# Performance work log

Measured on AMD Instinct MI355X. Metric: run time of the kernel, lower is better.

## Reference

```python
import jax, jax.numpy as jnp
import numpy as np


def setup_inputs() -> dict:
    key = jax.random.key(0)
    ks = jax.random.split(key, 5)
    bsz, input_size, hidden_size, level_hidden = 8192, 1024, 1024, 64
    d_in = input_size + hidden_size
    return {
        "input": jax.random.normal(ks[0], (bsz, input_size), dtype=jnp.float32),
        "h_prev": jax.random.normal(ks[1], (bsz, hidden_size), dtype=jnp.float32),
        "c_prev": jax.random.normal(ks[2], (bsz, hidden_size), dtype=jnp.float32),
        "W_lstm": jax.random.normal(ks[3], (4 * hidden_size, d_in), dtype=jnp.float32) * (1.0 / np.sqrt(d_in)),
        "W_level": jax.random.normal(ks[4], (2 * level_hidden, d_in), dtype=jnp.float32) * (1.0 / np.sqrt(d_in)),
    }


def reference(input, h_prev, c_prev, W_lstm, W_level):
    hidden_size = h_prev.shape[1]
    level_hidden = W_level.shape[0] // 2
    n_repeat = hidden_size // level_hidden

    combined = jnp.concatenate([input, h_prev], axis=-1)  # (B, in+hid)
    lstm_out = combined @ W_lstm.T                        # (B, 4*hid)
    cc_i, cc_f, cc_o, cc_g = jnp.split(lstm_out, 4, axis=1)
    level_out = combined @ W_level.T                      # (B, 2*lvl)
    cc_i_h, cc_f_h = jnp.split(level_out, 2, axis=1)

    i = jax.nn.sigmoid(cc_i)
    f = jax.nn.sigmoid(cc_f)
    o = jax.nn.sigmoid(cc_o)
    g = jnp.tanh(cc_g)

    p_f = jax.nn.softmax(cc_f_h, axis=-1)
    p_i = jax.nn.softmax(cc_i_h, axis=-1)
    f_h = jnp.cumsum(p_f, axis=-1)                         # forward cumsum
    i_h = jnp.flip(jnp.cumsum(jnp.flip(p_i, -1), axis=-1), -1)  # reverse cumsum

    # expand each level gate value across its chunk of the hidden dim
    i_h = jnp.repeat(i_h, n_repeat, axis=1)                # (B, hid)
    f_h = jnp.repeat(f_h, n_repeat, axis=1)

    w = i_h * f_h
    c = w * (f * c_prev + i * g) + (f_h - w) * c_prev + (i_h - w) * g
    h = o * jnp.tanh(c)
    return (h, c)
```

## Files before the change

### kernel.cpp

```cpp
#include <hip/hip_runtime.h>


typedef unsigned short u16;
typedef __attribute__((ext_vector_type(8))) short bf16x8;
typedef __attribute__((ext_vector_type(8))) short s8v;
typedef __attribute__((ext_vector_type(4))) float f32x4;
typedef __attribute__((ext_vector_type(4))) float v4f;

#define GLDS(g, l) __builtin_amdgcn_global_load_lds(                      \
    (const __attribute__((address_space(1))) void*)(g),                   \
    (__attribute__((address_space(3))) void*)(l), 16, 0, 0)

__device__ __forceinline__ u16 f2bf(float x) {
  unsigned u = __builtin_bit_cast(unsigned, x);
  u += 0x7FFFu + ((u >> 16) & 1u);
  return (u16)(u >> 16);
}
__device__ __forceinline__ float bf2f(u16 h) {
  unsigned u = ((unsigned)h) << 16;
  return __builtin_bit_cast(float, u);
}
__device__ __forceinline__ float fsig(float x) { return 1.0f / (1.0f + __expf(-x)); }
__device__ __forceinline__ float ftanhf(float x) { float e = __expf(2.0f * x); return 1.0f - 2.0f / (e + 1.0f); }

__global__ __launch_bounds__(256) void k_convert(
    const float* __restrict__ inp, const float* __restrict__ hprev,
    const float* __restrict__ wl, const float* __restrict__ wlev,
    u16* __restrict__ Ahi, u16* __restrict__ Alo,
    u16* __restrict__ Whi, u16* __restrict__ Wlo)
{
  const int GA = (8192 * 2048) / 8;
  const int GW = (4224 * 2048) / 8;
  for (int gi = blockIdx.x * 256 + threadIdx.x; gi < GA + GW; gi += gridDim.x * 256) {
    if (gi < GA) {
      int e = gi << 3; int row = e >> 11, col = e & 2047;
      const float* src = (col < 1024) ? (inp + row * 1024 + col)
                                      : (hprev + row * 1024 + (col - 1024));
      v4f a = *(const v4f*)src, b = *(const v4f*)(src + 4);
      float vv[8] = {a.x, a.y, a.z, a.w, b.x, b.y, b.z, b.w};
      s8v hi, lo;
#pragma unroll
      for (int j = 0; j < 8; ++j) {
        u16 h = f2bf(vv[j]);
        hi[j] = (short)h;
        lo[j] = (short)f2bf(vv[j] - bf2f(h));
      }
      *(s8v*)(Ahi + e) = hi;
      *(s8v*)(Alo + e) = lo;
    } else {
      int e = (gi - GA) << 3; int n = e >> 11, k = e & 2047;
      const float* src;
      if (n < 4096) { int j = n >> 2, g = n & 3; src = wl + (size_t)((g << 10) | j) * 2048 + k; }
      else          { src = wlev + (size_t)(n - 4096) * 2048 + k; }
      v4f a = *(const v4f*)src, b = *(const v4f*)(src + 4);
      float vv[8] = {a.x, a.y, a.z, a.w, b.x, b.y, b.z, b.w};
      s8v hi, lo;
#pragma unroll
      for (int j = 0; j < 8; ++j) {
        u16 h = f2bf(vv[j]);
        hi[j] = (short)h;
        lo[j] = (short)f2bf(vv[j] - bf2f(h));
      }
      *(s8v*)(Whi + e) = hi;
      if (n >= 4096) *(s8v*)(Wlo + (size_t)(n - 4096) * 2048 + k) = lo;
    }
  }
}

__global__ __launch_bounds__(256) void k_gemm_level(
    const u16* __restrict__ Ahi, const u16* __restrict__ Alo,
    const u16* __restrict__ Whi, const u16* __restrict__ Wlo,
    float* __restrict__ part)
{
  __shared__ __align__(16) u16 smem[4 * 8192];
  u16 *Ah = smem, *Al = smem + 8192, *Bh = smem + 16384, *Bl = smem + 24576;
  const int tid = threadIdx.x, lane = tid & 63, wid = tid >> 6;
  const int wm = wid >> 1, wn = wid & 1;
  const int rm = blockIdx.x, s = blockIdx.y;
  const int lrow = lane >> 3, lcolE = (lane & 7) << 3;
  const int c16 = lane & 15, r16 = lane >> 4;
  f32x4 acc[4][4] = {};
  const u16* aBaseH = Ahi + (size_t)(rm << 7) * 2048;
  const u16* aBaseL = Alo + (size_t)(rm << 7) * 2048;
  const u16* bBaseH = Whi + (size_t)4096 * 2048;

  for (int kt = 0; kt < 4; ++kt) {
    const int k0 = (s << 8) + (kt << 6);
#pragma unroll
    for (int q = 0; q < 4; ++q) {
      const int ca = (wid << 2) + q;
      size_t roff = (size_t)((ca << 3) + lrow) * 2048 + k0 + lcolE;
      GLDS(aBaseH + roff, Ah + (ca << 9));
      GLDS(aBaseL + roff, Al + (ca << 9));
      GLDS(bBaseH + roff, Bh + (ca << 9));
      GLDS(Wlo + roff,    Bl + (ca << 9));
    }
    __syncthreads();
#pragma unroll
    for (int ks = 0; ks < 2; ++ks) {
      bf16x8 ah[4], al[4];
#pragma unroll
      for (int i = 0; i < 4; ++i) {
        int off = ((wm << 6) + (i << 4) + c16) * 64 + (ks << 5) + (r16 << 3);
        ah[i] = *(const bf16x8*)(Ah + off);
        al[i] = *(const bf16x8*)(Al + off);
      }
#pragma unroll
      for (int j = 0; j < 4; ++j) {
        int off = ((wn << 6) + (j << 4) + c16) * 64 + (ks << 5) + (r16 << 3);
        bf16x8 bh = *(const bf16x8*)(Bh + off);
        bf16x8 bl = *(const bf16x8*)(Bl + off);
#pragma unroll
        for (int i = 0; i < 4; ++i) {
          acc[i][j] = __builtin_amdgcn_mfma_f32_16x16x32_bf16(ah[i], bh, acc[i][j], 0, 0, 0);
          acc[i][j] = __builtin_amdgcn_mfma_f32_16x16x32_bf16(al[i], bh, acc[i][j], 0, 0, 0);
          acc[i][j] = __builtin_amdgcn_mfma_f32_16x16x32_bf16(ah[i], bl, acc[i][j], 0, 0, 0);
        }
      }
    }
    __syncthreads();
  }
#pragma unroll
  for (int mi = 0; mi < 4; ++mi)
#pragma unroll
    for (int ni = 0; ni < 4; ++ni)
#pragma unroll
      for (int r = 0; r < 4; ++r) {
        int ml = (wm << 6) + (mi << 4) + (r16 << 2) + r;
        int nl = (wn << 6) + (ni << 4) + c16;
        part[(size_t)((s << 13) + (rm << 7) + ml) * 128 + nl] = acc[mi][ni][r];
      }
}

__global__ __launch_bounds__(256) void k_softmax(
    const float* __restrict__ part, float* __restrict__ ih, float* __restrict__ fh)
{
  const int tid = threadIdx.x, lane = tid & 63, w = tid >> 6;
  const int row = blockIdx.x * 4 + w;
  float vi = 0.f, vf = 0.f;
#pragma unroll
  for (int s = 0; s < 8; ++s) {
    vi += part[(size_t)((s << 13) + row) * 128 + lane];
    vf += part[(size_t)((s << 13) + row) * 128 + 64 + lane];
  }
  float mi = vi, mf = vf;
#pragma unroll
  for (int d = 1; d < 64; d <<= 1) {
    mi = fmaxf(mi, __shfl_xor(mi, d, 64));
    mf = fmaxf(mf, __shfl_xor(mf, d, 64));
  }
  float ei = __expf(vi - mi), ef = __expf(vf - mf);
  float si = ei, sf = ef;
#pragma unroll
  for (int d = 1; d < 64; d <<= 1) {
    si += __shfl_xor(si, d, 64);
    sf += __shfl_xor(sf, d, 64);
  }
  float pi = ei / si, pf = ef / sf;
  float ci = pi, cf = pf;
#pragma unroll
  for (int d = 1; d < 64; d <<= 1) {
    float t = __shfl_up(ci, d, 64); if (lane >= d) ci += t;
    float u = __shfl_up(cf, d, 64); if (lane >= d) cf += u;
  }
  ih[(row << 6) + lane] = 1.0f - (ci - pi);
  fh[(row << 6) + lane] = cf;
}

__global__ __launch_bounds__(512, 4) void k_gemm_main(
    const u16* __restrict__ Ab, const u16* __restrict__ Wb,
    const float* __restrict__ cprev, const float* __restrict__ ihp,
    const float* __restrict__ fhp, float* __restrict__ out)
{
  __shared__ __align__(16) u16 smem[36864];
  const int tid = threadIdx.x, lane = tid & 63, wid = tid >> 6;
  const int wm = wid >> 2, wn = wid & 3;
  const int c16 = lane & 15, r16 = lane >> 4;

  const int bx = blockIdx.x;
  const int nb = (bx & 7) * 128 + (bx >> 3);
  const int rm = nb >> 5, cm = nb & 31;

  const int sr = tid >> 2;
  const int slq = tid & 3;
  const int xk = (slq ^ ((sr >> 1) & 3)) << 3;
  const u16* pa = Ab + (size_t)(rm * 256 + sr) * 2048 + xk;
  const u16* pb = Wb + (size_t)(cm * 128 + sr) * 2048 + xk;
  char* const ldsW = (char*)smem + (wid << 10);

  const int xsl = (r16 ^ ((c16 >> 1) & 3)) << 3;
  const int base_a = (wm * 128 + c16) * 32 + xsl;
  const int base_b = 8192 + (wn * 32 + c16) * 32 + xsl;

  f32x4 acc[8][2] = {};

#define STAGE3(slice, slot) do {                                       \
    const u16* sa_ = pa + (slice) * 32;                                \
    const u16* sb_ = pb + (slice) * 32;                                \
    char* d_ = ldsW + (slot) * 24576;                                  \
    GLDS(sa_, d_); GLDS(sa_ + 262144, d_ + 8192);                      \
    GLDS(sb_, d_ + 16384);                                             \
  } while (0)

#define SLICE(s, slot, dostage) do {                                   \
    bf16x8 aX[8], bS[2];                                               \
    _Pragma("unroll")                                                  \
    for (int i = 0; i < 8; ++i)                                        \
      aX[i] = *(const bf16x8*)(smem + (slot) * 12288 + base_a + i * 512); \
    _Pragma("unroll")                                                  \
    for (int j = 0; j < 2; ++j)                                        \
      bS[j] = *(const bf16x8*)(smem + (slot) * 12288 + base_b + j * 512); \
    if (dostage) STAGE3(((s) + 2) & 63, ((s) + 2) % 3);                \
    asm volatile("s_waitcnt vmcnt(3)" ::: "memory");                   \
    __builtin_amdgcn_s_barrier();                                      \
    asm volatile("s_waitcnt lgkmcnt(0)" ::: "memory");                 \
    _Pragma("unroll")                                                  \
    for (int i = 0; i < 8; ++i)                                        \
      _Pragma("unroll")                                                \
      for (int j = 0; j < 2; ++j)                                      \
        acc[i][j] = __builtin_amdgcn_mfma_f32_16x16x32_bf16(           \
            aX[i], bS[j], acc[i][j], 0, 0, 0);                         \
    __builtin_amdgcn_s_barrier();                                      \
  } while (0)

  STAGE3(0, 0); STAGE3(1, 1);
  asm volatile("s_waitcnt vmcnt(3)" ::: "memory");
  __builtin_amdgcn_s_barrier();

  for (int u = 0; u < 21; ++u) {
    const int s0 = u * 3;
    SLICE(s0 + 0, 0, 1);
    SLICE(s0 + 1, 1, 1);
    SLICE(s0 + 2, 2, 1);
  }
  SLICE(63, 0, 0);
#undef SLICE
#undef STAGE3

  asm volatile("s_waitcnt vmcnt(0)" ::: "memory");
  __builtin_amdgcn_s_barrier();

  float* epi = (float*)smem;
#define EPIPASS(p) do {                                                \
    if (wm == (p)) {                                                   \
      _Pragma("unroll")                                                \
      for (int i = 0; i < 8; ++i)                                      \
        _Pragma("unroll")                                              \
        for (int j = 0; j < 2; ++j)                                    \
          _Pragma("unroll")                                            \
          for (int r = 0; r < 4; ++r) {                                \
            float v = acc[i][j][r];                                    \
            v = ((c16 & 3) == 3) ? ftanhf(v) : fsig(v);                \
            epi[(i * 16 + r16 * 4 + r) * 128 + wn * 32 + j * 16 + c16] = v; \
          }                                                            \
    }                                                                  \
    __syncthreads();                                                   \
    _Pragma("unroll")                                                  \
    for (int e = 0; e < 2; ++e) {                                      \
      int idx = (e << 9) + tid;                                        \
      int mrow = idx >> 3, q = idx & 7;                                \
      const float* g4 = epi + mrow * 128 + q * 16;                     \
      int rowg = rm * 256 + (p) * 128 + mrow;                          \
      int jgb = cm * 32 + q * 4;                                       \
      int lv = jgb >> 4;                                               \
      float vih = ihp[(rowg << 6) + lv], vfh = fhp[(rowg << 6) + lv];  \
      float wq = vih * vfh;                                            \
      v4f cp4 = *(const v4f*)(cprev + rowg * 1024 + jgb);              \
      float cpv[4] = {cp4.x, cp4.y, cp4.z, cp4.w};                     \
      v4f hv, cv;                                                      \
      _Pragma("unroll")                                                \
      for (int t = 0; t < 4; ++t) {                                    \
        v4f g = *(const v4f*)(g4 + t * 4);                             \
        float iv = g.x, fv = g.y, ov = g.z, gv = g.w;                  \
        float cpx = cpv[t];                                            \
        float c = wq * (fv * cpx + iv * gv) + (vfh - wq) * cpx + (vih - wq) * gv; \
        float h = ov * ftanhf(c);                                      \
        hv[t] = h; cv[t] = c;                                          \
      }                                                                \
      *(v4f*)(out + rowg * 1024 + jgb) = hv;                           \
      *(v4f*)(out + 8388608 + rowg * 1024 + jgb) = cv;                 \
    }                                                                  \
    __syncthreads();                                                   \
  } while (0)
  EPIPASS(0); EPIPASS(1);
#undef EPIPASS
}

extern "C" void kernel_launch(void* const* d_in, const int* in_sizes, int n_in,
                              void* d_out, int out_size, void* d_ws, size_t ws_size,
                              hipStream_t stream) {
  (void)in_sizes; (void)n_in; (void)out_size; (void)ws_size;
  const float* inp   = (const float*)d_in[0];
  const float* hprev = (const float*)d_in[1];
  const float* cprev = (const float*)d_in[2];
  const float* wl    = (const float*)d_in[3];
  const float* wlev  = (const float*)d_in[4];
  float* out = (float*)d_out;
  char* ws = (char*)d_ws;

  u16* Ahi  = (u16*)(ws);
  u16* Alo  = (u16*)(ws + 33554432);
  u16* Whi  = (u16*)(ws + 67108864);
  u16* Wlo  = (u16*)(ws + 84410368);
  float* part = (float*)(ws + 84934656);
  float* ih   = (float*)(ws + 118489088);
  float* fh   = (float*)(ws + 120586240);

  k_convert<<<dim3(2048), dim3(256), 0, stream>>>(inp, hprev, wl, wlev, Ahi, Alo, Whi, Wlo);
  k_gemm_level<<<dim3(64, 8), dim3(256), 0, stream>>>(Ahi, Alo, Whi, Wlo, part);
  k_softmax<<<dim3(2048), dim3(256), 0, stream>>>(part, ih, fh);
  k_gemm_main<<<dim3(1024), dim3(512), 0, stream>>>(Ahi, Whi, cprev, ih, fh, out);
}
```

Measured before the change: 224.2 us.

## Use 4-wave blocks with 128x64 warp tiles and double-buffered LDS register reads

Halves the main GEMM's threads per block from 512 to 256 and doubles each wave's tile to 8x4 MFMA blocks, so each A fragment read from LDS feeds four MFMAs instead of two. The loop is rewritten with two register sets (X/Y) so LDS reads for the next slice are issued before the MFMAs on the current slice, and each thread now issues six global-to-LDS loads per stage. This raises register pressure (64 accumulator vectors plus two fragment sets) and lowers waves per block, which risks spills or lower occupancy.

Measured after the change: 245.0 us. 1.09x slower.

```diff
diff --git a/kernel.cpp b/kernel.cpp
--- a/kernel.cpp
+++ b/kernel.cpp
@@ -167,14 +167,14 @@
   fh[(row << 6) + lane] = cf;
 }
 
-__global__ __launch_bounds__(512, 4) void k_gemm_main(
+__global__ __launch_bounds__(256, 2) void k_gemm_main(
     const u16* __restrict__ Ab, const u16* __restrict__ Wb,
     const float* __restrict__ cprev, const float* __restrict__ ihp,
     const float* __restrict__ fhp, float* __restrict__ out)
 {
   __shared__ __align__(16) u16 smem[36864];
   const int tid = threadIdx.x, lane = tid & 63, wid = tid >> 6;
-  const int wm = wid >> 2, wn = wid & 3;
+  const int wm = wid >> 1, wn = wid & 1;
   const int c16 = lane & 15, r16 = lane >> 4;
 
   const int bx = blockIdx.x;
@@ -190,55 +190,106 @@
 
   const int xsl = (r16 ^ ((c16 >> 1) & 3)) << 3;
   const int base_a = (wm * 128 + c16) * 32 + xsl;
-  const int base_b = 8192 + (wn * 32 + c16) * 32 + xsl;
-
-  f32x4 acc[8][2] = {};
-
-#define STAGE3(slice, slot) do {                                       \
+  const int base_b = 8192 + (wn * 64 + c16) * 32 + xsl;
+
+  f32x4 acc[8][4] = {};
+  bf16x8 aX0, aX1, aX2, aX3, aX4, aX5, aX6, aX7, bX0, bX1, bX2, bX3;
+  bf16x8 aY0, aY1, aY2, aY3, aY4, aY5, aY6, aY7, bY0, bY1, bY2, bY3;
+
+#define STAGE6(slice, slot) do {                                       \
     const u16* sa_ = pa + (slice) * 32;                                \
     const u16* sb_ = pb + (slice) * 32;                                \
     char* d_ = ldsW + (slot) * 24576;                                  \
-    GLDS(sa_, d_); GLDS(sa_ + 262144, d_ + 8192);                      \
-    GLDS(sb_, d_ + 16384);                                             \
-  } while (0)
-
-#define SLICE(s, slot, dostage) do {                                   \
-    bf16x8 aX[8], bS[2];                                               \
-    _Pragma("unroll")                                                  \
-    for (int i = 0; i < 8; ++i)                                        \
-      aX[i] = *(const bf16x8*)(smem + (slot) * 12288 + base_a + i * 512); \
-    _Pragma("unroll")                                                  \
-    for (int j = 0; j < 2; ++j)                                        \
-      bS[j] = *(const bf16x8*)(smem + (slot) * 12288 + base_b + j * 512); \
-    if (dostage) STAGE3(((s) + 2) & 63, ((s) + 2) % 3);                \
-    asm volatile("s_waitcnt vmcnt(3)" ::: "memory");                   \
-    __builtin_amdgcn_s_barrier();                                      \
-    asm volatile("s_waitcnt lgkmcnt(0)" ::: "memory");                 \
-    _Pragma("unroll")                                                  \
-    for (int i = 0; i < 8; ++i)                                        \
-      _Pragma("unroll")                                                \
-      for (int j = 0; j < 2; ++j)                                      \
-        acc[i][j] = __builtin_amdgcn_mfma_f32_16x16x32_bf16(           \
-            aX[i], bS[j], acc[i][j], 0, 0, 0);                         \
-    __builtin_amdgcn_s_barrier();                                      \
-  } while (0)
-
-  STAGE3(0, 0); STAGE3(1, 1);
-  asm volatile("s_waitcnt vmcnt(3)" ::: "memory");
-  __builtin_amdgcn_s_barrier();
-
-  for (int u = 0; u < 21; ++u) {
-    const int s0 = u * 3;
-    SLICE(s0 + 0, 0, 1);
-    SLICE(s0 + 1, 1, 1);
-    SLICE(s0 + 2, 2, 1);
-  }
-  SLICE(63, 0, 0);
-#undef SLICE
-#undef STAGE3
-
-  asm volatile("s_waitcnt vmcnt(0)" ::: "memory");
-  __builtin_amdgcn_s_barrier();
+    GLDS(sa_,          d_);                                            \
+    GLDS(sa_ + 131072, d_ + 4096);                                     \
+    GLDS(sa_ + 262144, d_ + 8192);                                     \
+    GLDS(sa_ + 393216, d_ + 12288);                                    \
+    GLDS(sb_,          d_ + 16384);                                    \
+    GLDS(sb_ + 131072, d_ + 20480);                                    \
+  } while (0)
+
+#define READX(slot) do {                                               \
+    const u16* p_ = smem + (slot) * 12288;                             \
+    aX0 = *(const bf16x8*)(p_ + base_a);                               \
+    aX1 = *(const bf16x8*)(p_ + base_a + 512);                         \
+    aX2 = *(const bf16x8*)(p_ + base_a + 1024);                        \
+    aX3 = *(const bf16x8*)(p_ + base_a + 1536);                        \
+    aX4 = *(const bf16x8*)(p_ + base_a + 2048);                        \
+    aX5 = *(const bf16x8*)(p_ + base_a + 2560);                        \
+    aX6 = *(const bf16x8*)(p_ + base_a + 3072);                        \
+    aX7 = *(const bf16x8*)(p_ + base_a + 3584);                        \
+    bX0 = *(const bf16x8*)(p_ + base_b);                               \
+    bX1 = *(const bf16x8*)(p_ + base_b + 512);                         \
+    bX2 = *(const bf16x8*)(p_ + base_b + 1024);                        \
+    bX3 = *(const bf16x8*)(p_ + base_b + 1536);                        \
+  } while (0)
+
+#define READY(slot) do {                                               \
+    const u16* p_ = smem + (slot) * 12288;                             \
+    aY0 = *(const bf16x8*)(p_ + base_a);                               \
+    aY1 = *(const bf16x8*)(p_ + base_a + 512);                         \
+    aY2 = *(const bf16x8*)(p_ + base_a + 1024);                        \
+    aY3 = *(const bf16x8*)(p_ + base_a + 1536);                        \
+    aY4 = *(const bf16x8*)(p_ + base_a + 2048);                        \
+    aY5 = *(const bf16x8*)(p_ + base_a + 2560);                        \
+    aY6 = *(const bf16x8*)(p_ + base_a + 3072);                        \
+    aY7 = *(const bf16x8*)(p_ + base_a + 3584);                        \
+    bY0 = *(const bf16x8*)(p_ + base_b);                               \
+    bY1 = *(const bf16x8*)(p_ + base_b + 512);                         \
+    bY2 = *(const bf16x8*)(p_ + base_b + 1024);                        \
+    bY3 = *(const bf16x8*)(p_ + base_b + 1536);                        \
+  } while (0)
+
+#define MM1(i_, A_)                                                    \
+    acc[i_][0] = __builtin_amdgcn_mfma_f32_16x16x32_bf16(A_, b_0, acc[i_][0], 0, 0, 0); \
+    acc[i_][1] = __builtin_amdgcn_mfma_f32_16x16x32_bf16(A_, b_1, acc[i_][1], 0, 0, 0); \
+    acc[i_][2] = __builtin_amdgcn_mfma_f32_16x16x32_bf16(A_, b_2, acc[i_][2], 0, 0, 0); \
+    acc[i_][3] = __builtin_amdgcn_mfma_f32_16x16x32_bf16(A_, b_3, acc[i_][3], 0, 0, 0);
+
+#define MFMAX() do {                                                   \
+    bf16x8 b_0 = bX0, b_1 = bX1, b_2 = bX2, b_3 = bX3;                 \
+    MM1(0, aX0) MM1(1, aX1) MM1(2, aX2) MM1(3, aX3)                    \
+    MM1(4, aX4) MM1(5, aX5) MM1(6, aX6) MM1(7, aX7)                    \
+  } while (0)
+
+#define MFMAY() do {                                                   \
+    bf16x8 b_0 = bY0, b_1 = bY1, b_2 = bY2, b_3 = bY3;                 \
+    MM1(0, aY0) MM1(1, aY1) MM1(2, aY2) MM1(3, aY3)                    \
+    MM1(4, aY4) MM1(5, aY5) MM1(6, aY6) MM1(7, aY7)                    \
+  } while (0)
+
+#define VM6() asm volatile("s_waitcnt vmcnt(6)" ::: "memory")
+#define VM0() asm volatile("s_waitcnt vmcnt(0)" ::: "memory")
+#define BAR() __builtin_amdgcn_s_barrier()
+
+  STAGE6(0, 0); STAGE6(1, 1);
+  VM6();
+  BAR();
+  READX(0);
+
+  for (int u = 0; u < 10; ++u) {
+    const int s0 = u * 6;
+    STAGE6(s0 + 2, 2); VM6(); BAR(); READY(1); MFMAX(); BAR();
+    STAGE6(s0 + 3, 0); VM6(); BAR(); READX(2); MFMAY(); BAR();
+    STAGE6(s0 + 4, 1); VM6(); BAR(); READY(0); MFMAX(); BAR();
+    STAGE6(s0 + 5, 2); VM6(); BAR(); READX(1); MFMAY(); BAR();
+    STAGE6(s0 + 6, 0); VM6(); BAR(); READY(2); MFMAX(); BAR();
+    STAGE6(s0 + 7, 1); VM6(); BAR(); READX(0); MFMAY(); BAR();
+  }
+  STAGE6(62, 2); VM6(); BAR(); READY(1); MFMAX(); BAR();
+  STAGE6(63, 0); VM6(); BAR(); READX(2); MFMAY(); BAR();
+  VM0(); BAR(); READY(0); MFMAX(); BAR();
+  MFMAY();
+  BAR();
+#undef STAGE6
+#undef READX
+#undef READY
+#undef MM1
+#undef MFMAX
+#undef MFMAY
+#undef VM6
+#undef VM0
+#undef BAR
 
   float* epi = (float*)smem;
 #define EPIPASS(p) do {                                                \
@@ -246,18 +297,18 @@
       _Pragma("unroll")                                                \
       for (int i = 0; i < 8; ++i)                                      \
         _Pragma("unroll")                                              \
-        for (int j = 0; j < 2; ++j)                                    \
+        for (int j = 0; j < 4; ++j)                                    \
           _Pragma("unroll")                                            \
           for (int r = 0; r < 4; ++r) {                                \
             float v = acc[i][j][r];                                    \
             v = ((c16 & 3) == 3) ? ftanhf(v) : fsig(v);                \
-            epi[(i * 16 + r16 * 4 + r) * 128 + wn * 32 + j * 16 + c16] = v; \
+            epi[(i * 16 + r16 * 4 + r) * 128 + wn * 64 + j * 16 + c16] = v; \
           }                                                            \
     }                                                                  \
     __syncthreads();                                                   \
     _Pragma("unroll")                                                  \
-    for (int e = 0; e < 2; ++e) {                                      \
-      int idx = (e << 9) + tid;                                        \
+    for (int e = 0; e < 4; ++e) {                                      \
+      int idx = (e << 8) + tid;                                        \
       int mrow = idx >> 3, q = idx & 7;                                \
       const float* g4 = epi + mrow * 128 + q * 16;                     \
       int rowg = rm * 256 + (p) * 128 + mrow;                          \
@@ -309,5 +360,5 @@
   k_convert<<<dim3(2048), dim3(256), 0, stream>>>(inp, hprev, wl, wlev, Ahi, Alo, Whi, Wlo);
   k_gemm_level<<<dim3(64, 8), dim3(256), 0, stream>>>(Ahi, Alo, Whi, Wlo, part);
   k_softmax<<<dim3(2048), dim3(256), 0, stream>>>(part, ih, fh);
-  k_gemm_main<<<dim3(1024), dim3(512), 0, stream>>>(Ahi, Whi, cprev, ih, fh, out);
-}
+  k_gemm_main<<<dim3(1024), dim3(256), 0, stream>>>(Ahi, Whi, cprev, ih, fh, out);
+}
```
